# Kernel tuning notes

Hardware: AMD Instinct MI355X
Metric: run time of the kernel (lower is better)

Reference implementation:

```python
import jax, jax.numpy as jnp
import numpy as np

D_MODEL = 1024
NUM_HEADS = 16
MAX_LEN = 2048
D_HEAD = D_MODEL // NUM_HEADS
BATCH = 2
SEQ = 2048


def setup_inputs() -> dict:
    key = jax.random.key(0)
    ks = jax.random.split(key, 8)
    s = 1.0 / np.sqrt(D_MODEL)
    return {
        "x": jax.random.normal(ks[0], (BATCH, SEQ, D_MODEL), dtype=jnp.float32),
        "Wq": jax.random.uniform(ks[1], (D_MODEL, D_MODEL), jnp.float32, -s, s),
        "bq": jax.random.uniform(ks[2], (D_MODEL,), jnp.float32, -s, s),
        "Wk": jax.random.uniform(ks[3], (D_MODEL, D_MODEL), jnp.float32, -s, s),
        "bk": jax.random.uniform(ks[4], (D_MODEL,), jnp.float32, -s, s),
        "Wv": jax.random.uniform(ks[5], (D_MODEL, D_MODEL), jnp.float32, -s, s),
        "bv": jax.random.uniform(ks[6], (D_MODEL,), jnp.float32, -s, s),
        "Er": jax.random.normal(ks[7], (MAX_LEN, D_HEAD), dtype=jnp.float32),
    }


def _skew(QEr):
    # QEr: [B, H, S, S]  (music-transformer skew trick)
    B, H, S, _ = QEr.shape
    padded = jnp.pad(QEr, ((0, 0), (0, 0), (0, 0), (1, 0)))  # [B,H,S,S+1]
    reshaped = padded.reshape(B, H, S + 1, S)
    return reshaped[:, :, 1:, :]  # [B,H,S,S]


def reference(x, Wq, bq, Wk, bk, Wv, bv, Er):
    B, S, D = x.shape
    H, Dh = NUM_HEADS, D_HEAD
    # projections (torch Linear: x @ W.T + b)
    q = (jnp.einsum('bsd,ed->bse', x, Wq) + bq).reshape(B, S, H, Dh).transpose(0, 2, 1, 3)
    k = (jnp.einsum('bsd,ed->bse', x, Wk) + bk).reshape(B, S, H, Dh).transpose(0, 2, 1, 3)
    v = (jnp.einsum('bsd,ed->bse', x, Wv) + bv).reshape(B, S, H, Dh).transpose(0, 2, 1, 3)
    # relative position scores
    Er_slice = Er[MAX_LEN - S:, :]                    # [S, Dh]
    QEr = jnp.einsum('bhsd,td->bhst', q, Er_slice)    # [B,H,S,S]
    Srel = _skew(QEr)
    QKt = jnp.einsum('bhsd,bhtd->bhst', q, k)
    attn = (QKt + Srel) / jnp.sqrt(jnp.asarray(Dh, x.dtype))
    causal = jnp.tril(jnp.ones((S, S), dtype=bool))
    attn = jnp.where(causal[None, None], attn, -jnp.inf)
    attn = jax.nn.softmax(attn, axis=-1)
    out = jnp.einsum('bhst,bhtd->bhsd', attn, v)      # [B,H,S,Dh]
    out = out.transpose(0, 2, 1, 3).reshape(B, S, D)
    return out  # dropout is identity in eval mode
```

## Files before the change

### kernel.cpp

```cpp
#include <hip/hip_runtime.h>
#include <hip/hip_bf16.h>

constexpr int B  = 2;
constexpr int S  = 2048;
constexpr int D  = 1024;
constexpr int H  = 16;

typedef unsigned short u16t;
typedef unsigned long long u64;
typedef __attribute__((ext_vector_type(8))) short short8;
typedef __attribute__((ext_vector_type(4))) float float4v;

__device__ __forceinline__ float b2f(unsigned int u) {
    union { unsigned int i; float f; } c; c.i = u << 16; return c.f;
}
__device__ __forceinline__ u16t f2b(float f) {
    __hip_bfloat16 h = __float2bfloat16(f);
    union { __hip_bfloat16 h; u16t u; } c; c.h = h; return c.u;
}
__device__ __forceinline__ unsigned int pkbf(float a, float b) {
    return (unsigned int)f2b(a) | ((unsigned int)f2b(b) << 16);
}
__device__ __forceinline__ u64 pack4(float4 v) {
    return (u64)f2b(v.x) | ((u64)f2b(v.y) << 16) | ((u64)f2b(v.z) << 32) | ((u64)f2b(v.w) << 48);
}

typedef __attribute__((address_space(1))) const unsigned int* as1_u32p;
typedef __attribute__((address_space(3))) unsigned int* as3_u32p;
__device__ __forceinline__ void gll16(const void* g, void* l) {
    __builtin_amdgcn_global_load_lds((as1_u32p)g, (as3_u32p)l, 16, 0, 0);
}

constexpr size_t XB_OFF = 0;
constexpr size_t WQ_OFF = 4194304;
constexpr size_t WK_OFF = 5242880;
constexpr size_t WV_OFF = 6291456;
constexpr size_t ER_OFF = 7340032;
constexpr size_t QW_OFF = 7471104;
constexpr size_t KW_OFF = 11665408;
constexpr size_t VT_OFF = 15859712;

__global__ __launch_bounds__(256) void prep_bf16(
    const float* __restrict__ x,  const float* __restrict__ Wq,
    const float* __restrict__ Wk, const float* __restrict__ Wv,
    const float* __restrict__ Er, u64* __restrict__ dst)
{
    size_t i4 = (size_t)blockIdx.x * 256 + threadIdx.x;
    const float* src; size_t off;
    if      (i4 < 1048576) { src = x;  off = i4; }
    else if (i4 < 1310720) { src = Wq; off = i4 - 1048576; }
    else if (i4 < 1572864) { src = Wk; off = i4 - 1310720; }
    else if (i4 < 1835008) { src = Wv; off = i4 - 1572864; }
    else                   { src = Er; off = i4 - 1835008; }
    float4 v = ((const float4*)src)[off];
    dst[i4] = pack4(v);
}

__global__ __launch_bounds__(256, 3) void qkv_mfma(
    const u16t* __restrict__ xb,
    const u16t* __restrict__ wqb, const u16t* __restrict__ wkb, const u16t* __restrict__ wvb,
    const float* __restrict__ bq, const float* __restrict__ bk, const float* __restrict__ bv,
    u16t* __restrict__ qo, u16t* __restrict__ ko, u16t* __restrict__ vT)
{
    const int z = blockIdx.z;
    const u16t*  W    = (z == 0) ? wqb : (z == 1) ? wkb : wvb;
    const float* bias = (z == 0) ? bq  : (z == 1) ? bk  : bv;

    __shared__ __align__(16) u16t SMEM[2 * 128 * 64];
    char* XsB = (char*)SMEM;
    char* WsB = XsB + 16384;

    const int tid = threadIdx.x;
    const int w = tid >> 6, lane = tid & 63;
    const int quad = lane >> 4, l16 = lane & 15;
    const int m0 = blockIdx.x * 128, n0 = blockIdx.y * 128;
    const int mi = (w >> 1) * 64, ni = (w & 1) * 64;

    const int srow = lane >> 3;
    const int d8s  = (lane & 7) ^ (srow & 7);
    const int xk   = l16 & 7;

    float4v acc[4][4];
    #pragma unroll
    for (int mt = 0; mt < 4; ++mt)
        #pragma unroll
        for (int nt = 0; nt < 4; ++nt) acc[mt][nt] = (float4v){0.f, 0.f, 0.f, 0.f};

    for (int k0 = 0; k0 < D; k0 += 64) {
        #pragma unroll
        for (int it = 0; it < 4; ++it) {
            int ci  = w * 4 + it;
            int row = ci * 8 + srow;
            gll16(&xb[(size_t)(m0 + row) * D + k0 + d8s * 8], XsB + ci * 1024);
            gll16(&W [(size_t)(n0 + row) * D + k0 + d8s * 8], WsB + ci * 1024);
        }
        __syncthreads();

        short8 af[4][2], bf[4][2];
        #pragma unroll
        for (int mt = 0; mt < 4; ++mt) {
            int r = mi + mt * 16 + l16;
            af[mt][0] = *(const short8*)(XsB + r * 128 + ((quad       ^ xk) << 4));
            af[mt][1] = *(const short8*)(XsB + r * 128 + (((quad + 4) ^ xk) << 4));
        }
        #pragma unroll
        for (int nt = 0; nt < 4; ++nt) {
            int r = ni + nt * 16 + l16;
            bf[nt][0] = *(const short8*)(WsB + r * 128 + ((quad       ^ xk) << 4));
            bf[nt][1] = *(const short8*)(WsB + r * 128 + (((quad + 4) ^ xk) << 4));
        }
        #pragma unroll
        for (int mt = 0; mt < 4; ++mt)
            #pragma unroll
            for (int nt = 0; nt < 4; ++nt) {
                acc[mt][nt] = __builtin_amdgcn_mfma_f32_16x16x32_bf16(af[mt][0], bf[nt][0], acc[mt][nt], 0, 0, 0);
                acc[mt][nt] = __builtin_amdgcn_mfma_f32_16x16x32_bf16(af[mt][1], bf[nt][1], acc[mt][nt], 0, 0, 0);
            }
        __syncthreads();
    }

    float bias_v[4];
    #pragma unroll
    for (int nt = 0; nt < 4; ++nt) bias_v[nt] = bias[n0 + ni + nt * 16 + l16];
    #pragma unroll
    for (int mt = 0; mt < 4; ++mt)
        #pragma unroll
        for (int nt = 0; nt < 4; ++nt)
            #pragma unroll
            for (int rg = 0; rg < 4; ++rg) acc[mt][nt][rg] += bias_v[nt];

    const int hB = n0 >> 6;
    const int b_ = m0 >> 11;
    const int sB = m0 & (S - 1);
    char* EP = (char*)SMEM;

    if (z < 2) {
        u16t* outp = (z == 0) ? qo : ko;
        #pragma unroll 1
        for (int hp = 0; hp < 2; ++hp) {
            __syncthreads();
            if ((w & 1) == hp) {
                #pragma unroll
                for (int mt = 0; mt < 4; ++mt)
                    #pragma unroll
                    for (int nt = 0; nt < 4; ++nt) {
                        int col = nt * 16 + l16;
                        #pragma unroll
                        for (int rg = 0; rg < 4; ++rg) {
                            int row = mi + mt * 16 + quad * 4 + rg;
                            *(u16t*)(EP + row * 144 + col * 2) = f2b(acc[mt][nt][rg]);
                        }
                    }
            }
            __syncthreads();
            #pragma unroll
            for (int it = 0; it < 4; ++it) {
                int idx = tid + it * 256;
                int row = idx >> 3, c8 = idx & 7;
                short8 vv = *(const short8*)(EP + row * 144 + c8 * 16);
                *(short8*)&outp[((size_t)(b_ * H + hB + hp) * S + sB + row) * 64 + c8 * 8] = vv;
            }
        }
    } else {
        #pragma unroll 1
        for (int hp = 0; hp < 2; ++hp) {
            __syncthreads();
            if ((w & 1) == hp) {
                #pragma unroll
                for (int mt = 0; mt < 4; ++mt)
                    #pragma unroll
                    for (int nt = 0; nt < 4; ++nt) {
                        int rowD = nt * 16 + l16;
                        #pragma unroll
                        for (int rg = 0; rg < 4; ++rg) {
                            int colS = mi + mt * 16 + quad * 4 + rg;
                            *(u16t*)(EP + rowD * 272 + colS * 2) = f2b(acc[mt][nt][rg]);
                        }
                    }
            }
            __syncthreads();
            #pragma unroll
            for (int it = 0; it < 4; ++it) {
                int idx = tid + it * 256;
                int rowD = idx >> 4, c16 = idx & 15;
                short8 vv = *(const short8*)(EP + rowD * 272 + c16 * 16);
                *(short8*)&vT[((size_t)(b_ * H + hB + hp) * 64 + rowD) * S + sB + c16 * 8] = vv;
            }
        }
    }
}

__global__ __launch_bounds__(256, 4) void attn_mfma(
    const u16t* __restrict__ q, const u16t* __restrict__ k,
    const u16t* __restrict__ vT, const u16t* __restrict__ er,
    float* __restrict__ out)
{
    __shared__ __align__(16) u16t KsS[2][64 * 64];
    __shared__ __align__(16) u16t VsS[2][64 * 64];
    __shared__ __align__(16) u16t PsS[64 * 64];
    char* KsB = (char*)KsS;
    char* VsB = (char*)VsS;
    char* PsB = (char*)PsS;
    float* lrows = (float*)PsS;

    const int tid = threadIdx.x;
    const int w = tid >> 6, lane = tid & 63;
    const int quad = lane >> 4, l16 = lane & 15;

    const int r_  = blockIdx.x;
    const int g   = blockIdx.y;
    const int bh  = r_ & 31;
    const int slot = r_ >> 5;
    const int ix  = (g == 0) ? (31 - slot)
                  : (g == 1) ? (16 + slot)
                  : (g == 2) ? (15 - slot)
                  :            slot;
    const int hh = bh & (H - 1), bb = bh >> 4;

    const u16t* qb = q  + (size_t)bh * S * 64;
    const u16t* kb = k  + (size_t)bh * S * 64;
    const u16t* vb = vT + (size_t)bh * 64 * S;

    const int xk = (l16 & 7);
    const float SC = 0.18033688f;
    const float M2 = 17.3125f;

    const int srow = lane >> 3;
    const int d8s  = (lane & 7) ^ (srow & 7);

    const int s0 = ix * 64;

    const size_t qoff = (size_t)(s0 + w * 16 + l16) * 64;
    const short8 Qa0 = *(const short8*)&qb[qoff + quad * 8];
    const short8 Qa1 = *(const short8*)&qb[qoff + 32 + quad * 8];

    float4v accO[4], L[5];
    #pragma unroll
    for (int t = 0; t < 4; ++t) accO[t] = (float4v){0.f, 0.f, 0.f, 0.f};
    float lsum[4] = {0.f, 0.f, 0.f, 0.f};

    #pragma unroll
    for (int it = 0; it < 2; ++it) {
        int ci = w * 2 + it;
        int prow = ci * 8 + srow;
        gll16(&kb[(size_t)prow * 64 + d8s * 8], KsB + ci * 1024);
        gll16(&vb[(size_t)prow * S + d8s * 8], VsB + ci * 1024);
    }
    __syncthreads();

    for (int jt = 0; jt <= ix; ++jt) {
        const int t0 = jt * 64;
        const int jbase = S - 64 - s0 + t0;
        const bool diag = (jt == ix);
        const int bsel = (jt & 1) * 8192;

        short8 ef0[4], ef1[4], e00, e01;
        #pragma unroll
        for (int c = 1; c <= 4; ++c) {
            int grow = jbase + (3 - w + c) * 16 + l16;
            if (grow > S - 1) grow = S - 1;
            const u16t* ep = &er[(size_t)grow * 64 + quad * 8];
            ef0[c - 1] = *(const short8*)ep;
            ef1[c - 1] = *(const short8*)(ep + 32);
        }
        if (jt == 0) {
            int grow = jbase + (3 - w) * 16 + l16;
            if (grow > S - 1) grow = S - 1;
            const u16t* ep = &er[(size_t)grow * 64 + quad * 8];
            e00 = *(const short8*)ep;
            e01 = *(const short8*)(ep + 32);
        }

        if (jt < ix) {
            int nb = ((jt + 1) & 1) * 8192;
            #pragma unroll
            for (int it = 0; it < 2; ++it) {
                int ci = w * 2 + it;
                int prow = ci * 8 + srow;
                gll16(&kb[(size_t)(t0 + 64 + prow) * 64 + d8s * 8], KsB + nb + ci * 1024);
                gll16(&vb[(size_t)prow * S + t0 + 64 + d8s * 8], VsB + nb + ci * 1024);
            }
        }

        __builtin_amdgcn_s_setprio(1);
        float4v S1[4];
        #pragma unroll
        for (int nt = 0; nt < 4; ++nt) {
            int row = nt * 16 + l16;
            short8 b0 = *(const short8*)(KsB + bsel + row * 128 + ((quad ^ xk) << 4));
            short8 b1 = *(const short8*)(KsB + bsel + row * 128 + (((quad + 4) ^ xk) << 4));
            float4v a = (float4v){0.f, 0.f, 0.f, 0.f};
            a = __builtin_amdgcn_mfma_f32_16x16x32_bf16(Qa0, b0, a, 0, 0, 0);
            a = __builtin_amdgcn_mfma_f32_16x16x32_bf16(Qa1, b1, a, 0, 0, 0);
            S1[nt] = a;
        }

        if (jt == 0) {
            float4v e = (float4v){0.f, 0.f, 0.f, 0.f};
            e = __builtin_amdgcn_mfma_f32_16x16x32_bf16(Qa0, e00, e, 0, 0, 0);
            e = __builtin_amdgcn_mfma_f32_16x16x32_bf16(Qa1, e01, e, 0, 0, 0);
            L[0] = e;
        } else {
            L[0] = L[4];
        }
        #pragma unroll
        for (int c = 1; c <= 4; ++c) {
            float4v e = (float4v){0.f, 0.f, 0.f, 0.f};
            e = __builtin_amdgcn_mfma_f32_16x16x32_bf16(Qa0, ef0[c - 1], e, 0, 0, 0);
            e = __builtin_amdgcn_mfma_f32_16x16x32_bf16(Qa1, ef1[c - 1], e, 0, 0, 0);
            L[c] = e;
        }
        __builtin_amdgcn_s_setprio(0);

        #pragma unroll
        for (int rg = 0; rg < 4; ++rg) {
            const int usel = quad * 4 + rg;
            const int thr = 15 - usel;
            const int sidx = ((lane & 48) | ((l16 + thr) & 15)) * 4;
            const bool give_lo = (l16 >= thr);
            unsigned int p01 = give_lo ? pkbf(L[0][rg], L[1][rg]) : pkbf(L[1][rg], L[2][rg]);
            unsigned int p23 = give_lo ? pkbf(L[2][rg], L[3][rg]) : pkbf(L[3][rg], L[4][rg]);
            unsigned int q01 = (unsigned int)__builtin_amdgcn_ds_bpermute(sidx, (int)p01);
            unsigned int q23 = (unsigned int)__builtin_amdgcn_ds_bpermute(sidx, (int)p23);
            float qe[4] = { b2f(q01 & 0xffffu), b2f(q01 >> 16),
                            b2f(q23 & 0xffffu), b2f(q23 >> 16) };
            const int i_ = w * 16 + usel;
            const int ikey = i_ & 7;
            float psum = 0.f;
            #pragma unroll
            for (int nt = 0; nt < 4; ++nt) {
                float s2 = fmaf(S1[nt][rg] + qe[nt], SC, -M2);
                float p = (diag && (nt * 16 + l16 > i_)) ? 0.f : exp2f(s2);
                psum += p;
                int j_ = nt * 16 + l16;
                *(u16t*)(PsB + i_ * 128 + (((j_ >> 3) ^ ikey) << 4) + (j_ & 7) * 2) = f2b(p);
            }
            lsum[rg] += psum;
        }

        {
            __builtin_amdgcn_s_setprio(1);
            int ar = w * 16 + l16;
            short8 pa0 = *(const short8*)(PsB + ar * 128 + ((quad ^ (ar & 7)) << 4));
            short8 pa1 = *(const short8*)(PsB + ar * 128 + (((quad + 4) ^ (ar & 7)) << 4));
            #pragma unroll
            for (int td = 0; td < 4; ++td) {
                int row = td * 16 + l16;
                short8 a0 = *(const short8*)(VsB + bsel + row * 128 + ((quad ^ xk) << 4));
                short8 a1 = *(const short8*)(VsB + bsel + row * 128 + (((quad + 4) ^ xk) << 4));
                accO[td] = __builtin_amdgcn_mfma_f32_16x16x32_bf16(a0, pa0, accO[td], 0, 0, 0);
                accO[td] = __builtin_amdgcn_mfma_f32_16x16x32_bf16(a1, pa1, accO[td], 0, 0, 0);
            }
            __builtin_amdgcn_s_setprio(0);
        }
        __syncthreads();
    }

    #pragma unroll
    for (int rg = 0; rg < 4; ++rg) {
        float s = lsum[rg];
        s += __shfl_xor(s, 1);
        s += __shfl_xor(s, 2);
        s += __shfl_xor(s, 4);
        s += __shfl_xor(s, 8);
        if (l16 == 0) lrows[w * 16 + quad * 4 + rg] = s;
    }
    float inv = 1.f / lrows[w * 16 + l16];

    float* ob = out + (size_t)bb * S * D + (size_t)hh * 64
                + (size_t)(s0 + w * 16 + l16) * D;
    #pragma unroll
    for (int td = 0; td < 4; ++td) {
        float4 o;
        o.x = accO[td][0] * inv;
        o.y = accO[td][1] * inv;
        o.z = accO[td][2] * inv;
        o.w = accO[td][3] * inv;
        *(float4*)&ob[td * 16 + quad * 4] = o;
    }
}

extern "C" void kernel_launch(void* const* d_in, const int* in_sizes, int n_in,
                              void* d_out, int out_size, void* d_ws, size_t ws_size,
                              hipStream_t stream) {
    const float* x  = (const float*)d_in[0];
    const float* Wq = (const float*)d_in[1];
    const float* bq = (const float*)d_in[2];
    const float* Wk = (const float*)d_in[3];
    const float* bk = (const float*)d_in[4];
    const float* Wv = (const float*)d_in[5];
    const float* bv = (const float*)d_in[6];
    const float* Er = (const float*)d_in[7];
    float* out = (float*)d_out;

    u16t* ws16 = (u16t*)d_ws;
    u16t* xb  = ws16 + XB_OFF;
    u16t* wqb = ws16 + WQ_OFF;
    u16t* wkb = ws16 + WK_OFF;
    u16t* wvb = ws16 + WV_OFF;
    u16t* erb = ws16 + ER_OFF;
    u16t* qw  = ws16 + QW_OFF;
    u16t* kw  = ws16 + KW_OFF;
    u16t* vTw = ws16 + VT_OFF;

    prep_bf16<<<dim3(7296), dim3(256), 0, stream>>>(x, Wq, Wk, Wv, Er, (u64*)d_ws);

    qkv_mfma<<<dim3(32, 8, 3), dim3(256), 0, stream>>>(
        xb, wqb, wkb, wvb, bq, bk, bv, qw, kw, vTw);

    attn_mfma<<<dim3(256, 4), dim3(256), 0, stream>>>(qw, kw, vTw, erb, out);
}
```

Before: 200.7 us.

## Use 128-row query tiles with 8 waves sharing K/V tiles in attention

The attention kernel now runs 512-thread blocks covering 128 query rows (8 waves), so each K/V tile loaded into LDS serves twice as many query rows. This halves global K/V traffic per query. Each wave loads one chunk per tile, and the first four waves skip the final diagonal tile, which lies fully above their rows. The grid shrinks to 256x2 with a simpler pairing for load balance, the setprio hints are dropped, and LDS per block grows, which may reduce occupancy.

```diff
diff --git a/kernel.cpp b/kernel.cpp
--- a/kernel.cpp
+++ b/kernel.cpp
@@ -190,14 +190,14 @@
     }
 }
 
-__global__ __launch_bounds__(256, 4) void attn_mfma(
+__global__ __launch_bounds__(512, 4) void attn_mfma(
     const u16t* __restrict__ q, const u16t* __restrict__ k,
     const u16t* __restrict__ vT, const u16t* __restrict__ er,
     float* __restrict__ out)
 {
     __shared__ __align__(16) u16t KsS[2][64 * 64];
     __shared__ __align__(16) u16t VsS[2][64 * 64];
-    __shared__ __align__(16) u16t PsS[64 * 64];
+    __shared__ __align__(16) u16t PsS[128 * 64];
     char* KsB = (char*)KsS;
     char* VsB = (char*)VsS;
     char* PsB = (char*)PsS;
@@ -207,14 +207,12 @@
     const int w = tid >> 6, lane = tid & 63;
     const int quad = lane >> 4, l16 = lane & 15;
 
-    const int r_  = blockIdx.x;
-    const int g   = blockIdx.y;
-    const int bh  = r_ & 31;
+    const int r_   = blockIdx.x;
+    const int g    = blockIdx.y;
+    const int bh   = r_ & 31;
     const int slot = r_ >> 5;
-    const int ix  = (g == 0) ? (31 - slot)
-                  : (g == 1) ? (16 + slot)
-                  : (g == 2) ? (15 - slot)
-                  :            slot;
+    const int qt   = g ? slot : (15 - slot);
+    const int jmax = 2 * qt + 1;
     const int hh = bh & (H - 1), bb = bh >> 4;
 
     const u16t* qb = q  + (size_t)bh * S * 64;
@@ -227,8 +225,9 @@
 
     const int srow = lane >> 3;
     const int d8s  = (lane & 7) ^ (srow & 7);
-
-    const int s0 = ix * 64;
+    const int prow = w * 8 + srow;
+
+    const int s0 = qt * 128;
 
     const size_t qoff = (size_t)(s0 + w * 16 + l16) * 64;
     const short8 Qa0 = *(const short8*)&qb[qoff + quad * 8];
@@ -239,119 +238,110 @@
     for (int t = 0; t < 4; ++t) accO[t] = (float4v){0.f, 0.f, 0.f, 0.f};
     float lsum[4] = {0.f, 0.f, 0.f, 0.f};
 
-    #pragma unroll
-    for (int it = 0; it < 2; ++it) {
-        int ci = w * 2 + it;
-        int prow = ci * 8 + srow;
-        gll16(&kb[(size_t)prow * 64 + d8s * 8], KsB + ci * 1024);
-        gll16(&vb[(size_t)prow * S + d8s * 8], VsB + ci * 1024);
-    }
+    gll16(&kb[(size_t)prow * 64 + d8s * 8], KsB + w * 1024);
+    gll16(&vb[(size_t)prow * S + d8s * 8], VsB + w * 1024);
     __syncthreads();
 
-    for (int jt = 0; jt <= ix; ++jt) {
+    for (int jt = 0; jt <= jmax; ++jt) {
         const int t0 = jt * 64;
         const int jbase = S - 64 - s0 + t0;
-        const bool diag = (jt == ix);
+        const bool diag  = (t0 >= s0);
+        const int  joff  = t0 - s0;
+        const bool skipc = (jt == jmax) && (w < 4);
         const int bsel = (jt & 1) * 8192;
 
-        short8 ef0[4], ef1[4], e00, e01;
-        #pragma unroll
-        for (int c = 1; c <= 4; ++c) {
-            int grow = jbase + (3 - w + c) * 16 + l16;
-            if (grow > S - 1) grow = S - 1;
-            const u16t* ep = &er[(size_t)grow * 64 + quad * 8];
-            ef0[c - 1] = *(const short8*)ep;
-            ef1[c - 1] = *(const short8*)(ep + 32);
-        }
-        if (jt == 0) {
-            int grow = jbase + (3 - w) * 16 + l16;
-            if (grow > S - 1) grow = S - 1;
-            const u16t* ep = &er[(size_t)grow * 64 + quad * 8];
-            e00 = *(const short8*)ep;
-            e01 = *(const short8*)(ep + 32);
-        }
-
-        if (jt < ix) {
+        if (jt < jmax) {
             int nb = ((jt + 1) & 1) * 8192;
-            #pragma unroll
-            for (int it = 0; it < 2; ++it) {
-                int ci = w * 2 + it;
-                int prow = ci * 8 + srow;
-                gll16(&kb[(size_t)(t0 + 64 + prow) * 64 + d8s * 8], KsB + nb + ci * 1024);
-                gll16(&vb[(size_t)prow * S + t0 + 64 + d8s * 8], VsB + nb + ci * 1024);
-            }
-        }
-
-        __builtin_amdgcn_s_setprio(1);
-        float4v S1[4];
-        #pragma unroll
-        for (int nt = 0; nt < 4; ++nt) {
-            int row = nt * 16 + l16;
-            short8 b0 = *(const short8*)(KsB + bsel + row * 128 + ((quad ^ xk) << 4));
-            short8 b1 = *(const short8*)(KsB + bsel + row * 128 + (((quad + 4) ^ xk) << 4));
-            float4v a = (float4v){0.f, 0.f, 0.f, 0.f};
-            a = __builtin_amdgcn_mfma_f32_16x16x32_bf16(Qa0, b0, a, 0, 0, 0);
-            a = __builtin_amdgcn_mfma_f32_16x16x32_bf16(Qa1, b1, a, 0, 0, 0);
-            S1[nt] = a;
-        }
-
-        if (jt == 0) {
-            float4v e = (float4v){0.f, 0.f, 0.f, 0.f};
-            e = __builtin_amdgcn_mfma_f32_16x16x32_bf16(Qa0, e00, e, 0, 0, 0);
-            e = __builtin_amdgcn_mfma_f32_16x16x32_bf16(Qa1, e01, e, 0, 0, 0);
-            L[0] = e;
-        } else {
-            L[0] = L[4];
-        }
-        #pragma unroll
-        for (int c = 1; c <= 4; ++c) {
-            float4v e = (float4v){0.f, 0.f, 0.f, 0.f};
-            e = __builtin_amdgcn_mfma_f32_16x16x32_bf16(Qa0, ef0[c - 1], e, 0, 0, 0);
-            e = __builtin_amdgcn_mfma_f32_16x16x32_bf16(Qa1, ef1[c - 1], e, 0, 0, 0);
-            L[c] = e;
-        }
-        __builtin_amdgcn_s_setprio(0);
-
-        #pragma unroll
-        for (int rg = 0; rg < 4; ++rg) {
-            const int usel = quad * 4 + rg;
-            const int thr = 15 - usel;
-            const int sidx = ((lane & 48) | ((l16 + thr) & 15)) * 4;
-            const bool give_lo = (l16 >= thr);
-            unsigned int p01 = give_lo ? pkbf(L[0][rg], L[1][rg]) : pkbf(L[1][rg], L[2][rg]);
-            unsigned int p23 = give_lo ? pkbf(L[2][rg], L[3][rg]) : pkbf(L[3][rg], L[4][rg]);
-            unsigned int q01 = (unsigned int)__builtin_amdgcn_ds_bpermute(sidx, (int)p01);
-            unsigned int q23 = (unsigned int)__builtin_amdgcn_ds_bpermute(sidx, (int)p23);
-            float qe[4] = { b2f(q01 & 0xffffu), b2f(q01 >> 16),
-                            b2f(q23 & 0xffffu), b2f(q23 >> 16) };
-            const int i_ = w * 16 + usel;
-            const int ikey = i_ & 7;
-            float psum = 0.f;
+            gll16(&kb[(size_t)(t0 + 64 + prow) * 64 + d8s * 8], KsB + nb + w * 1024);
+            gll16(&vb[(size_t)prow * S + t0 + 64 + d8s * 8], VsB + nb + w * 1024);
+        }
+
+        if (!skipc) {
+            short8 ef0[4], ef1[4], e00, e01;
+            #pragma unroll
+            for (int c = 1; c <= 4; ++c) {
+                int grow = jbase + (3 - w + c) * 16 + l16;
+                if (grow > S - 1) grow = S - 1;
+                const u16t* ep = &er[(size_t)grow * 64 + quad * 8];
+                ef0[c - 1] = *(const short8*)ep;
+                ef1[c - 1] = *(const short8*)(ep + 32);
+            }
+            if (jt == 0) {
+                int grow = jbase + (3 - w) * 16 + l16;
+                if (grow > S - 1) grow = S - 1;
+                if (grow < 0) grow = 0;
+                const u16t* ep = &er[(size_t)grow * 64 + quad * 8];
+                e00 = *(const short8*)ep;
+                e01 = *(const short8*)(ep + 32);
+            }
+
+            float4v S1[4];
             #pragma unroll
             for (int nt = 0; nt < 4; ++nt) {
-                float s2 = fmaf(S1[nt][rg] + qe[nt], SC, -M2);
-                float p = (diag && (nt * 16 + l16 > i_)) ? 0.f : exp2f(s2);
-                psum += p;
-                int j_ = nt * 16 + l16;
-                *(u16t*)(PsB + i_ * 128 + (((j_ >> 3) ^ ikey) << 4) + (j_ & 7) * 2) = f2b(p);
-            }
-            lsum[rg] += psum;
-        }
-
-        {
-            __builtin_amdgcn_s_setprio(1);
-            int ar = w * 16 + l16;
-            short8 pa0 = *(const short8*)(PsB + ar * 128 + ((quad ^ (ar & 7)) << 4));
-            short8 pa1 = *(const short8*)(PsB + ar * 128 + (((quad + 4) ^ (ar & 7)) << 4));
-            #pragma unroll
-            for (int td = 0; td < 4; ++td) {
-                int row = td * 16 + l16;
-                short8 a0 = *(const short8*)(VsB + bsel + row * 128 + ((quad ^ xk) << 4));
-                short8 a1 = *(const short8*)(VsB + bsel + row * 128 + (((quad + 4) ^ xk) << 4));
-                accO[td] = __builtin_amdgcn_mfma_f32_16x16x32_bf16(a0, pa0, accO[td], 0, 0, 0);
-                accO[td] = __builtin_amdgcn_mfma_f32_16x16x32_bf16(a1, pa1, accO[td], 0, 0, 0);
-            }
-            __builtin_amdgcn_s_setprio(0);
+                int row = nt * 16 + l16;
+                short8 b0 = *(const short8*)(KsB + bsel + row * 128 + ((quad ^ xk) << 4));
+                short8 b1 = *(const short8*)(KsB + bsel + row * 128 + (((quad + 4) ^ xk) << 4));
+                float4v a = (float4v){0.f, 0.f, 0.f, 0.f};
+                a = __builtin_amdgcn_mfma_f32_16x16x32_bf16(Qa0, b0, a, 0, 0, 0);
+                a = __builtin_amdgcn_mfma_f32_16x16x32_bf16(Qa1, b1, a, 0, 0, 0);
+                S1[nt] = a;
+            }
+
+            if (jt == 0) {
+                float4v e = (float4v){0.f, 0.f, 0.f, 0.f};
+                e = __builtin_amdgcn_mfma_f32_16x16x32_bf16(Qa0, e00, e, 0, 0, 0);
+                e = __builtin_amdgcn_mfma_f32_16x16x32_bf16(Qa1, e01, e, 0, 0, 0);
+                L[0] = e;
+            } else {
+                L[0] = L[4];
+            }
+            #pragma unroll
+            for (int c = 1; c <= 4; ++c) {
+                float4v e = (float4v){0.f, 0.f, 0.f, 0.f};
+                e = __builtin_amdgcn_mfma_f32_16x16x32_bf16(Qa0, ef0[c - 1], e, 0, 0, 0);
+                e = __builtin_amdgcn_mfma_f32_16x16x32_bf16(Qa1, ef1[c - 1], e, 0, 0, 0);
+                L[c] = e;
+            }
+
+            #pragma unroll
+            for (int rg = 0; rg < 4; ++rg) {
+                const int usel = quad * 4 + rg;
+                const int thr = 15 - usel;
+                const int sidx = ((lane & 48) | ((l16 + thr) & 15)) * 4;
+                const bool give_lo = (l16 >= thr);
+                unsigned int p01 = give_lo ? pkbf(L[0][rg], L[1][rg]) : pkbf(L[1][rg], L[2][rg]);
+                unsigned int p23 = give_lo ? pkbf(L[2][rg], L[3][rg]) : pkbf(L[3][rg], L[4][rg]);
+                unsigned int q01 = (unsigned int)__builtin_amdgcn_ds_bpermute(sidx, (int)p01);
+                unsigned int q23 = (unsigned int)__builtin_amdgcn_ds_bpermute(sidx, (int)p23);
+                float qe[4] = { b2f(q01 & 0xffffu), b2f(q01 >> 16),
+                                b2f(q23 & 0xffffu), b2f(q23 >> 16) };
+                const int i_ = w * 16 + usel;
+                const int ikey = i_ & 7;
+                float psum = 0.f;
+                #pragma unroll
+                for (int nt = 0; nt < 4; ++nt) {
+                    float s2 = fmaf(S1[nt][rg] + qe[nt], SC, -M2);
+                    float p = (diag && (joff + nt * 16 + l16 > i_)) ? 0.f : exp2f(s2);
+                    psum += p;
+                    int j_ = nt * 16 + l16;
+                    *(u16t*)(PsB + i_ * 128 + (((j_ >> 3) ^ ikey) << 4) + (j_ & 7) * 2) = f2b(p);
+                }
+                lsum[rg] += psum;
+            }
+
+            {
+                int ar = w * 16 + l16;
+                short8 pa0 = *(const short8*)(PsB + ar * 128 + ((quad ^ (ar & 7)) << 4));
+                short8 pa1 = *(const short8*)(PsB + ar * 128 + (((quad + 4) ^ (ar & 7)) << 4));
+                #pragma unroll
+                for (int td = 0; td < 4; ++td) {
+                    int row = td * 16 + l16;
+                    short8 a0 = *(const short8*)(VsB + bsel + row * 128 + ((quad ^ xk) << 4));
+                    short8 a1 = *(const short8*)(VsB + bsel + row * 128 + (((quad + 4) ^ xk) << 4));
+                    accO[td] = __builtin_amdgcn_mfma_f32_16x16x32_bf16(a0, pa0, accO[td], 0, 0, 0);
+                    accO[td] = __builtin_amdgcn_mfma_f32_16x16x32_bf16(a1, pa1, accO[td], 0, 0, 0);
+                }
+            }
         }
         __syncthreads();
     }
@@ -408,5 +398,5 @@
     qkv_mfma<<<dim3(32, 8, 3), dim3(256), 0, stream>>>(
         xb, wqb, wkb, wvb, bq, bk, bv, qw, kw, vTw);
 
-    attn_mfma<<<dim3(256, 4), dim3(256), 0, stream>>>(qw, kw, vTw, erb, out);
-}
+    attn_mfma<<<dim3(256, 2), dim3(512), 0, stream>>>(qw, kw, vTw, erb, out);
+}
```

Result: slower. 238.6 us (+18.9%).

## Read K/V tiles directly from global memory instead of LDS double buffering

Applied to the files above, without the earlier changes.

Drops the double-buffered async global-to-LDS staging of the K and V tiles. Each wave now loads its MFMA operands straight from global memory, relying on the caches. Because each wave only touches its own rows of the P tile, the per-iteration block barrier and the priority hints are removed, and the row-sum buffer gets its own small shared array. This cuts LDS use and synchronisation, which may raise occupancy, at the cost of each of the four waves fetching the same K/V data from global/L2 with exposed latency.

```diff
diff --git a/kernel.cpp b/kernel.cpp
--- a/kernel.cpp
+++ b/kernel.cpp
@@ -195,13 +195,9 @@
     const u16t* __restrict__ vT, const u16t* __restrict__ er,
     float* __restrict__ out)
 {
-    __shared__ __align__(16) u16t KsS[2][64 * 64];
-    __shared__ __align__(16) u16t VsS[2][64 * 64];
     __shared__ __align__(16) u16t PsS[64 * 64];
-    char* KsB = (char*)KsS;
-    char* VsB = (char*)VsS;
     char* PsB = (char*)PsS;
-    float* lrows = (float*)PsS;
+    __shared__ float lrows[64];
 
     const int tid = threadIdx.x;
     const int w = tid >> 6, lane = tid & 63;
@@ -221,12 +217,8 @@
     const u16t* kb = k  + (size_t)bh * S * 64;
     const u16t* vb = vT + (size_t)bh * 64 * S;
 
-    const int xk = (l16 & 7);
     const float SC = 0.18033688f;
     const float M2 = 17.3125f;
-
-    const int srow = lane >> 3;
-    const int d8s  = (lane & 7) ^ (srow & 7);
 
     const int s0 = ix * 64;
 
@@ -238,21 +230,11 @@
     #pragma unroll
     for (int t = 0; t < 4; ++t) accO[t] = (float4v){0.f, 0.f, 0.f, 0.f};
     float lsum[4] = {0.f, 0.f, 0.f, 0.f};
-
-    #pragma unroll
-    for (int it = 0; it < 2; ++it) {
-        int ci = w * 2 + it;
-        int prow = ci * 8 + srow;
-        gll16(&kb[(size_t)prow * 64 + d8s * 8], KsB + ci * 1024);
-        gll16(&vb[(size_t)prow * S + d8s * 8], VsB + ci * 1024);
-    }
-    __syncthreads();
 
     for (int jt = 0; jt <= ix; ++jt) {
         const int t0 = jt * 64;
         const int jbase = S - 64 - s0 + t0;
         const bool diag = (jt == ix);
-        const int bsel = (jt & 1) * 8192;
 
         short8 ef0[4], ef1[4], e00, e01;
         #pragma unroll
@@ -271,24 +253,12 @@
             e01 = *(const short8*)(ep + 32);
         }
 
-        if (jt < ix) {
-            int nb = ((jt + 1) & 1) * 8192;
-            #pragma unroll
-            for (int it = 0; it < 2; ++it) {
-                int ci = w * 2 + it;
-                int prow = ci * 8 + srow;
-                gll16(&kb[(size_t)(t0 + 64 + prow) * 64 + d8s * 8], KsB + nb + ci * 1024);
-                gll16(&vb[(size_t)prow * S + t0 + 64 + d8s * 8], VsB + nb + ci * 1024);
-            }
-        }
-
-        __builtin_amdgcn_s_setprio(1);
         float4v S1[4];
         #pragma unroll
         for (int nt = 0; nt < 4; ++nt) {
-            int row = nt * 16 + l16;
-            short8 b0 = *(const short8*)(KsB + bsel + row * 128 + ((quad ^ xk) << 4));
-            short8 b1 = *(const short8*)(KsB + bsel + row * 128 + (((quad + 4) ^ xk) << 4));
+            const u16t* kr = &kb[(size_t)(t0 + nt * 16 + l16) * 64];
+            short8 b0 = *(const short8*)(kr + quad * 8);
+            short8 b1 = *(const short8*)(kr + 32 + quad * 8);
             float4v a = (float4v){0.f, 0.f, 0.f, 0.f};
             a = __builtin_amdgcn_mfma_f32_16x16x32_bf16(Qa0, b0, a, 0, 0, 0);
             a = __builtin_amdgcn_mfma_f32_16x16x32_bf16(Qa1, b1, a, 0, 0, 0);
@@ -310,7 +280,6 @@
             e = __builtin_amdgcn_mfma_f32_16x16x32_bf16(Qa1, ef1[c - 1], e, 0, 0, 0);
             L[c] = e;
         }
-        __builtin_amdgcn_s_setprio(0);
 
         #pragma unroll
         for (int rg = 0; rg < 4; ++rg) {
@@ -339,21 +308,18 @@
         }
 
         {
-            __builtin_amdgcn_s_setprio(1);
             int ar = w * 16 + l16;
             short8 pa0 = *(const short8*)(PsB + ar * 128 + ((quad ^ (ar & 7)) << 4));
             short8 pa1 = *(const short8*)(PsB + ar * 128 + (((quad + 4) ^ (ar & 7)) << 4));
             #pragma unroll
             for (int td = 0; td < 4; ++td) {
-                int row = td * 16 + l16;
-                short8 a0 = *(const short8*)(VsB + bsel + row * 128 + ((quad ^ xk) << 4));
-                short8 a1 = *(const short8*)(VsB + bsel + row * 128 + (((quad + 4) ^ xk) << 4));
+                const u16t* vr = &vb[(size_t)(td * 16 + l16) * S + t0];
+                short8 a0 = *(const short8*)(vr + quad * 8);
+                short8 a1 = *(const short8*)(vr + 32 + quad * 8);
                 accO[td] = __builtin_amdgcn_mfma_f32_16x16x32_bf16(a0, pa0, accO[td], 0, 0, 0);
                 accO[td] = __builtin_amdgcn_mfma_f32_16x16x32_bf16(a1, pa1, accO[td], 0, 0, 0);
             }
-            __builtin_amdgcn_s_setprio(0);
-        }
-        __syncthreads();
+        }
     }
 
     #pragma unroll
```

New measurement: 295.3 us. +47.1%, slower.
